# Performance work log

Measured on AMD Instinct MI355X. Metric: run time of the kernel, lower is better.

## Reference

```python
import jax, jax.numpy as jnp
import numpy as np

B, S, IN_DIM = 8, 1024, 512
EMBED_DIM, NUM_HEADS = 512, 8
HEAD_DIM = EMBED_DIM // NUM_HEADS
LN_EPS = 1e-5


def setup_inputs() -> dict:
    key = jax.random.key(0)
    k1, k2, k3 = jax.random.split(key, 3)
    x = jax.random.normal(k1, (B, S, IN_DIM), dtype=jnp.float32)
    # xavier_uniform for qkv_proj.weight [3*embed, in] and o_proj.weight [embed, embed]
    lim_qkv = float(np.sqrt(6.0 / (3 * EMBED_DIM + IN_DIM)))
    w_qkv = jax.random.uniform(k2, (3 * EMBED_DIM, IN_DIM), dtype=jnp.float32,
                               minval=-lim_qkv, maxval=lim_qkv)
    lim_o = float(np.sqrt(6.0 / (EMBED_DIM + EMBED_DIM)))
    w_o = jax.random.uniform(k3, (EMBED_DIM, EMBED_DIM), dtype=jnp.float32,
                             minval=-lim_o, maxval=lim_o)
    return {"x": x, "w_qkv": w_qkv, "w_o": w_o}


def reference(x, w_qkv, w_o):
    b, s, _ = x.shape
    # fused QKV projection: [b, s, 3*embed]
    qkv = jnp.einsum('bsi,ei->bse', x, w_qkv)
    # [b, h, s, 3*head_dim]
    qkv = qkv.reshape(b, s, NUM_HEADS, 3 * HEAD_DIM).transpose(0, 2, 1, 3)
    q, k, v = jnp.split(qkv, 3, axis=-1)
    scale = 1.0 / np.sqrt(HEAD_DIM)
    logits = jnp.einsum('bhqd,bhkd->bhqk', q, k) * scale  # [b, h, s, s]
    attn = jax.nn.softmax(logits, axis=-1)
    vals = jnp.einsum('bhqk,bhkd->bhqd', attn, v)
    vals = vals.transpose(0, 2, 1, 3).reshape(b, s, EMBED_DIM)
    o = jnp.einsum('bse,fe->bsf', vals, w_o)
    # LayerNorm over [seq, embed] jointly (fresh nn.LayerNorm([N, D]): weight=1, bias=0)
    mu = jnp.mean(o, axis=(-2, -1), keepdims=True)
    var = jnp.var(o, axis=(-2, -1), keepdims=True)
    o = (o - mu) / jnp.sqrt(var + LN_EPS)
    return o
```

## Files before the change

### kernel.cpp

```cpp
#include <hip/hip_runtime.h>
#include <hip/hip_bf16.h>
#include <math.h>

#define BB 8
#define SS 1024
#define INDIM 512
#define ED 512
#define NH 8
#define HD 64

typedef __attribute__((ext_vector_type(8))) short short8;
typedef __attribute__((ext_vector_type(4))) float f32x4;
typedef __attribute__((ext_vector_type(16))) float f32x16;
typedef unsigned short u16;

typedef __attribute__((address_space(1))) const void gv_t;
typedef __attribute__((address_space(3))) void lv_t;

static __device__ __forceinline__ u16 f2bf(float f) {
  union { float f; unsigned u; } v; v.f = f;
  unsigned r = v.u + 0x7fffu + ((v.u >> 16) & 1u);
  return (u16)(r >> 16);
}
static __device__ __forceinline__ float bf2f(u16 b) {
  union { unsigned u; float f; } v; v.u = (unsigned)b << 16; return v.f;
}

static __device__ __forceinline__ unsigned cvt_pk_bf16(float a, float b) {
  unsigned r;
  asm("v_cvt_pk_bf16_f32 %0, %1, %2" : "=v"(r) : "v"(a), "v"(b));
  return r;
}
static __device__ __forceinline__ float fast_exp2(float x) {
  float r; asm("v_exp_f32 %0, %1" : "=v"(r) : "v"(x)); return r;
}

__global__ void cvt_all(const float* __restrict__ x, const float* __restrict__ wq,
                        const float* __restrict__ wo, u16* __restrict__ xb,
                        u16* __restrict__ wqb, u16* __restrict__ wob) {
  const int n1 = 1048576;
  const int n2 = n1 + 196608;
  const int n3 = n2 + 65536;
  int i = blockIdx.x * blockDim.x + threadIdx.x;
  int stride = gridDim.x * blockDim.x;
  for (; i < n3; i += stride) {
    const float4* src; ushort4* dst; int j;
    if (i < n1)      { src = (const float4*)x;  dst = (ushort4*)xb;  j = i; }
    else if (i < n2) { src = (const float4*)wq; dst = (ushort4*)wqb; j = i - n1; }
    else             { src = (const float4*)wo; dst = (ushort4*)wob; j = i - n2; }
    float4 v = src[j];
    ushort4 o;
    o.x = f2bf(v.x); o.y = f2bf(v.y); o.z = f2bf(v.z); o.w = f2bf(v.w);
    dst[j] = o;
  }
}

template<int EPI>
__global__ __launch_bounds__(256, 2)
void gemm_nt(const u16* __restrict__ A, const u16* __restrict__ Bm, int K,
             u16* __restrict__ outB,
             u16* __restrict__ qws, u16* __restrict__ kws, u16* __restrict__ vtws,
             float2* __restrict__ partials)
{
  __shared__ u16 As[128][64];
  __shared__ u16 Bs[128][64];
  const int tid = threadIdx.x;
  const int lane = tid & 63;
  const int wv = tid >> 6;
  const int wr = wv >> 1, wc = wv & 1;
  const int bm = blockIdx.x, bn = blockIdx.y;
  const int l15 = lane & 15, lg = lane >> 4;
  const int srow8 = lane >> 3;
  const int sc8 = lane & 7;

  f32x4 acc[4][4];
  #pragma unroll
  for (int i = 0; i < 4; i++)
    #pragma unroll
    for (int j = 0; j < 4; j++) acc[i][j] = (f32x4){0.f, 0.f, 0.f, 0.f};

  for (int kk = 0; kk < K; kk += 64) {
    #pragma unroll
    for (int i = 0; i < 4; i++) {
      int r0 = (i * 4 + wv) * 8;
      int r = r0 + srow8;
      int cs = sc8 ^ (r & 7);
      const u16* ga = A + (size_t)(bm * 128 + r) * K + kk + cs * 8;
      __builtin_amdgcn_global_load_lds((gv_t*)ga, (lv_t*)&As[r0][0], 16, 0, 0);
      const u16* gb = Bm + (size_t)(bn * 128 + r) * K + kk + cs * 8;
      __builtin_amdgcn_global_load_lds((gv_t*)gb, (lv_t*)&Bs[r0][0], 16, 0, 0);
    }
    __syncthreads();
    #pragma unroll
    for (int kc = 0; kc < 2; kc++) {
      short8 af[4], bf[4];
      #pragma unroll
      for (int mi = 0; mi < 4; mi++) {
        int ra = wr * 64 + mi * 16 + l15;
        af[mi] = *(const short8*)&As[ra][((kc * 4 + lg) ^ (ra & 7)) * 8];
      }
      #pragma unroll
      for (int ni = 0; ni < 4; ni++) {
        int rb = wc * 64 + ni * 16 + l15;
        bf[ni] = *(const short8*)&Bs[rb][((kc * 4 + lg) ^ (rb & 7)) * 8];
      }
      #pragma unroll
      for (int mi = 0; mi < 4; mi++)
        #pragma unroll
        for (int ni = 0; ni < 4; ni++)
          acc[mi][ni] = __builtin_amdgcn_mfma_f32_16x16x32_bf16(af[mi], bf[ni], acc[mi][ni], 0, 0, 0);
    }
    __syncthreads();
  }

  if (EPI == 0) {
    #pragma unroll
    for (int mi = 0; mi < 4; mi++) {
      int rowg = bm * 128 + wr * 64 + mi * 16 + lg * 4;
      #pragma unroll
      for (int ni = 0; ni < 4; ni++) {
        int colg = bn * 128 + wc * 64 + ni * 16 + l15;
        #pragma unroll
        for (int r = 0; r < 4; r++) {
          int rg = rowg + r;
          float v = acc[mi][ni][r];
          int b = rg >> 10, s = rg & 1023;
          int h = colg / 192, c = colg - h * 192;
          int bh = b * 8 + h;
          if (c < 64)
            qws[((size_t)(bh * 1024 + s)) * 64 + c] = f2bf(v * 0.18033688f);
          else if (c < 128)
            kws[((size_t)(bh * 1024 + s)) * 64 + (c - 64)] = f2bf(v);
          else
            vtws[((size_t)(bh * 64 + (c - 128))) * 1024 + s] = f2bf(v);
        }
      }
    }
  } else {
    float s1 = 0.f, s2 = 0.f;
    #pragma unroll
    for (int mi = 0; mi < 4; mi++) {
      int rowg = bm * 128 + wr * 64 + mi * 16 + lg * 4;
      #pragma unroll
      for (int ni = 0; ni < 4; ni++) {
        int colg = bn * 128 + wc * 64 + ni * 16 + l15;
        #pragma unroll
        for (int r = 0; r < 4; r++) {
          float v = acc[mi][ni][r];
          s1 += v; s2 += v * v;
          outB[(size_t)(rowg + r) * 512 + colg] = f2bf(v);
        }
      }
    }
    #pragma unroll
    for (int off = 1; off < 64; off <<= 1) {
      s1 += __shfl_xor(s1, off);
      s2 += __shfl_xor(s2, off);
    }
    __shared__ float r1[4], r2[4];
    if (lane == 0) { r1[wv] = s1; r2[wv] = s2; }
    __syncthreads();
    if (tid == 0) {
      float t1 = r1[0] + r1[1] + r1[2] + r1[3];
      float t2 = r2[0] + r2[1] + r2[2] + r2[3];
      partials[bm * 4 + bn] = make_float2(t1, t2);
    }
  }
}

__global__ __launch_bounds__(512, 4)
void attn_kernel(const u16* __restrict__ qws, const u16* __restrict__ kws,
                 const u16* __restrict__ vtws, u16* __restrict__ vals)
{
  __shared__ __align__(16) u16 Ksm[2][64][72];
  __shared__ __align__(16) u16 Vsm[2][64][72];
  const int tid = threadIdx.x;
  const int lane = tid & 63;
  const int wq = tid >> 6;
  const int l31 = lane & 31;
  const int hi = lane >> 5;
  const int logical = (blockIdx.x & 7) * 32 + (blockIdx.x >> 3);
  const int bh = logical >> 2;
  const int q0 = (logical & 3) * 256;

  short8 qf[4];
  {
    const u16* qp = qws + ((size_t)bh * 1024 + q0 + wq * 32 + l31) * 64 + 8 * hi;
    #pragma unroll
    for (int j = 0; j < 4; j++) qf[j] = *(const short8*)(qp + 16 * j);
  }

  const int srow = tid >> 3;
  const int sc8 = (tid & 7) * 8;
  uint4 kreg, vreg;
  kreg = *(const uint4*)(kws + ((size_t)bh * 1024 + srow) * 64 + sc8);
  vreg = *(const uint4*)(vtws + ((size_t)(bh * 64 + srow)) * 1024 + sc8);
  *(uint4*)&Ksm[0][srow][sc8] = kreg;
  *(uint4*)&Vsm[0][srow][sc8] = vreg;
  __syncthreads();

  f32x16 o[2];
  #pragma unroll
  for (int r = 0; r < 16; r++) { o[0][r] = 0.f; o[1][r] = 0.f; }
  float m = -1e30f, l = 0.f;

  for (int t = 0; t < 16; t++) {
    const int cur = t & 1;
    if (t < 15) {
      int kv = (t + 1) * 64;
      kreg = *(const uint4*)(kws + ((size_t)bh * 1024 + kv + srow) * 64 + sc8);
      vreg = *(const uint4*)(vtws + ((size_t)(bh * 64 + srow)) * 1024 + kv + sc8);
    }

    f32x16 stv[2];
    __builtin_amdgcn_s_setprio(1);
    #pragma unroll
    for (int s2 = 0; s2 < 2; s2++) {
      f32x16 c;
      #pragma unroll
      for (int r = 0; r < 16; r++) c[r] = 0.f;
      #pragma unroll
      for (int j = 0; j < 4; j++) {
        short8 kf = *(const short8*)&Ksm[cur][s2 * 32 + l31][16 * j + 8 * hi];
        c = __builtin_amdgcn_mfma_f32_32x32x16_bf16(kf, qf[j], c, 0, 0, 0);
      }
      stv[s2] = c;
    }
    __builtin_amdgcn_s_setprio(0);

    float mx[16];
    #pragma unroll
    for (int r = 0; r < 16; r++) mx[r] = fmaxf(stv[0][r], stv[1][r]);
    #pragma unroll
    for (int w = 8; w >= 1; w >>= 1)
      #pragma unroll
      for (int r = 0; r < w; r++) mx[r] = fmaxf(mx[r], mx[r + w]);
    float pm = fmaxf(mx[0], __shfl_xor(mx[0], 32));

    if (!__all(pm - m <= 10.0f)) {
      float mn = fmaxf(m, pm);
      float al = fast_exp2(m - mn);
      m = mn; l *= al;
      #pragma unroll
      for (int reg = 0; reg < 16; reg++) {
        int qrow = (reg & 3) + 8 * (reg >> 2) + 4 * hi;
        float alo = __shfl(al, qrow);
        o[0][reg] *= alo; o[1][reg] *= alo;
      }
    }

    unsigned pk[16];
    float ps[16];
    #pragma unroll
    for (int s2 = 0; s2 < 2; s2++)
      #pragma unroll
      for (int j = 0; j < 8; j++) {
        float p0 = fast_exp2(stv[s2][2 * j] - m);
        float p1 = fast_exp2(stv[s2][2 * j + 1] - m);
        ps[s2 * 8 + j] = p0 + p1;
        pk[s2 * 8 + j] = cvt_pk_bf16(p0, p1);
      }
    #pragma unroll
    for (int w = 8; w >= 1; w >>= 1)
      #pragma unroll
      for (int r = 0; r < w; r++) ps[r] += ps[r + w];
    l += ps[0] + __shfl_xor(ps[0], 32);

    short8 pa[4];
    #pragma unroll
    for (int cc = 0; cc < 4; cc++) {
      int base = (cc >> 1) * 8 + (cc & 1) * 4;
      unsigned a0 = pk[base + 0], a2 = pk[base + 2];
      unsigned a1 = pk[base + 1], a3 = pk[base + 3];
      asm volatile("v_permlane32_swap_b32 %0, %1" : "+v"(a0), "+v"(a2));
      asm volatile("v_permlane32_swap_b32 %0, %1" : "+v"(a1), "+v"(a3));
      union { unsigned u[4]; short8 s8; } uu;
      uu.u[0] = a0; uu.u[1] = a1; uu.u[2] = a2; uu.u[3] = a3;
      pa[cc] = uu.s8;
    }

    __builtin_amdgcn_s_setprio(1);
    #pragma unroll
    for (int dh = 0; dh < 2; dh++)
      #pragma unroll
      for (int cc = 0; cc < 4; cc++) {
        short8 vf = *(const short8*)&Vsm[cur][dh * 32 + l31][16 * cc + 8 * hi];
        o[dh] = __builtin_amdgcn_mfma_f32_32x32x16_bf16(pa[cc], vf, o[dh], 0, 0, 0);
      }
    __builtin_amdgcn_s_setprio(0);

    if (t < 15) {
      *(uint4*)&Ksm[cur ^ 1][srow][sc8] = kreg;
      *(uint4*)&Vsm[cur ^ 1][srow][sc8] = vreg;
    }
    __syncthreads();
  }

  const int b = bh >> 3, h = bh & 7;
  #pragma unroll
  for (int reg = 0; reg < 16; reg++) {
    int qrow = (reg & 3) + 8 * (reg >> 2) + 4 * hi;
    float linv = 1.0f / __shfl(l, qrow);
    size_t grow = (size_t)(b * 1024 + q0 + wq * 32 + qrow) * 512 + h * 64;
    vals[grow + l31]      = f2bf(o[0][reg] * linv);
    vals[grow + 32 + l31] = f2bf(o[1][reg] * linv);
  }
}

__global__ void ln_norm3(const u16* __restrict__ ob, float* __restrict__ o,
                         const float2* __restrict__ partials) {
  const int blk = blockIdx.x;
  const int b = blk >> 8;
  const int lane = threadIdx.x & 63;
  float s1 = 0.f, s2 = 0.f;
  if (lane < 32) {
    float2 p = partials[b * 32 + lane];
    s1 = p.x; s2 = p.y;
  }
  #pragma unroll
  for (int off = 1; off < 64; off <<= 1) {
    s1 += __shfl_xor(s1, off);
    s2 += __shfl_xor(s2, off);
  }
  float mu = s1 / 524288.f;
  float rs = rsqrtf(s2 / 524288.f - mu * mu + 1e-5f);
  const size_t i = (size_t)blk * 2048 + threadIdx.x * 8;
  uint4 v = *(const uint4*)(ob + i);
  float4 o0, o1;
  o0.x = (bf2f((u16)(v.x & 0xffff)) - mu) * rs;
  o0.y = (bf2f((u16)(v.x >> 16)) - mu) * rs;
  o0.z = (bf2f((u16)(v.y & 0xffff)) - mu) * rs;
  o0.w = (bf2f((u16)(v.y >> 16)) - mu) * rs;
  o1.x = (bf2f((u16)(v.z & 0xffff)) - mu) * rs;
  o1.y = (bf2f((u16)(v.z >> 16)) - mu) * rs;
  o1.z = (bf2f((u16)(v.w & 0xffff)) - mu) * rs;
  o1.w = (bf2f((u16)(v.w >> 16)) - mu) * rs;
  *(float4*)(o + i) = o0;
  *(float4*)(o + i + 4) = o1;
}

extern "C" void kernel_launch(void* const* d_in, const int* in_sizes, int n_in,
                              void* d_out, int out_size, void* d_ws, size_t ws_size,
                              hipStream_t stream) {
  const float* x = (const float*)d_in[0];
  const float* wqkv = (const float*)d_in[1];
  const float* wo = (const float*)d_in[2];
  float* out = (float*)d_out;
  char* ws = (char*)d_ws;

  u16* xb        = (u16*)(ws + 0);
  u16* wqb       = (u16*)(ws + 8388608);
  u16* wob       = (u16*)(ws + 9961472);
  u16* qws       = (u16*)(ws + 10485760);
  u16* kws       = (u16*)(ws + 18874368);
  u16* vtws      = (u16*)(ws + 27262976);
  u16* vals      = (u16*)(ws + 35651584);
  u16* outb      = (u16*)(ws + 44040192);
  float2* parts  = (float2*)(ws + 52428800);

  cvt_all<<<1280, 256, 0, stream>>>(x, wqkv, wo, xb, wqb, wob);

  dim3 g1(64, 12);
  gemm_nt<0><<<g1, 256, 0, stream>>>(xb, wqb, 512, nullptr, qws, kws, vtws, nullptr);

  attn_kernel<<<256, 512, 0, stream>>>(qws, kws, vtws, vals);

  dim3 g2(64, 4);
  gemm_nt<1><<<g2, 256, 0, stream>>>(vals, wob, 512, outb, nullptr, nullptr, nullptr, parts);

  ln_norm3<<<2048, 256, 0, stream>>>(outb, out, parts);
}
```

Measured before the change: 81.63 us.

## Double-buffer GEMM LDS tiles with K=32 steps to overlap loads and MFMA

Restructures the projection GEMM main loop so shared-memory tiles are double-buffered. The K step drops from 64 to 32 and the swizzle changes to match. The next tile is fetched with global_load_lds while MFMAs run on the current one, which removes the serialized load-then-compute pattern and one barrier per iteration. The trade-off is smaller K chunks per iteration and a lower MFMA-to-barrier ratio, and the smaller swizzle pattern may raise LDS bank conflicts.

```diff
diff --git a/kernel.cpp b/kernel.cpp
--- a/kernel.cpp
+++ b/kernel.cpp
@@ -62,16 +62,16 @@
              u16* __restrict__ qws, u16* __restrict__ kws, u16* __restrict__ vtws,
              float2* __restrict__ partials)
 {
-  __shared__ u16 As[128][64];
-  __shared__ u16 Bs[128][64];
+  __shared__ u16 As[2][128][32];
+  __shared__ u16 Bs[2][128][32];
   const int tid = threadIdx.x;
   const int lane = tid & 63;
   const int wv = tid >> 6;
   const int wr = wv >> 1, wc = wv & 1;
   const int bm = blockIdx.x, bn = blockIdx.y;
   const int l15 = lane & 15, lg = lane >> 4;
-  const int srow8 = lane >> 3;
-  const int sc8 = lane & 7;
+  const int srow16 = lane >> 2;
+  const int sc4 = lane & 3;
 
   f32x4 acc[4][4];
   #pragma unroll
@@ -79,37 +79,50 @@
     #pragma unroll
     for (int j = 0; j < 4; j++) acc[i][j] = (f32x4){0.f, 0.f, 0.f, 0.f};
 
-  for (int kk = 0; kk < K; kk += 64) {
-    #pragma unroll
-    for (int i = 0; i < 4; i++) {
-      int r0 = (i * 4 + wv) * 8;
-      int r = r0 + srow8;
-      int cs = sc8 ^ (r & 7);
-      const u16* ga = A + (size_t)(bm * 128 + r) * K + kk + cs * 8;
-      __builtin_amdgcn_global_load_lds((gv_t*)ga, (lv_t*)&As[r0][0], 16, 0, 0);
-      const u16* gb = Bm + (size_t)(bn * 128 + r) * K + kk + cs * 8;
-      __builtin_amdgcn_global_load_lds((gv_t*)gb, (lv_t*)&Bs[r0][0], 16, 0, 0);
-    }
-    __syncthreads();
-    #pragma unroll
-    for (int kc = 0; kc < 2; kc++) {
-      short8 af[4], bf[4];
-      #pragma unroll
-      for (int mi = 0; mi < 4; mi++) {
-        int ra = wr * 64 + mi * 16 + l15;
-        af[mi] = *(const short8*)&As[ra][((kc * 4 + lg) ^ (ra & 7)) * 8];
-      }
-      #pragma unroll
-      for (int ni = 0; ni < 4; ni++) {
-        int rb = wc * 64 + ni * 16 + l15;
-        bf[ni] = *(const short8*)&Bs[rb][((kc * 4 + lg) ^ (rb & 7)) * 8];
-      }
-      #pragma unroll
-      for (int mi = 0; mi < 4; mi++)
-        #pragma unroll
-        for (int ni = 0; ni < 4; ni++)
-          acc[mi][ni] = __builtin_amdgcn_mfma_f32_16x16x32_bf16(af[mi], bf[ni], acc[mi][ni], 0, 0, 0);
-    }
+  #pragma unroll
+  for (int i = 0; i < 2; i++) {
+    int r0 = (i * 4 + wv) * 16;
+    int r = r0 + srow16;
+    int cs = sc4 ^ (r & 3);
+    const u16* ga = A + (size_t)(bm * 128 + r) * K + cs * 8;
+    __builtin_amdgcn_global_load_lds((gv_t*)ga, (lv_t*)&As[0][r0][0], 16, 0, 0);
+    const u16* gb = Bm + (size_t)(bn * 128 + r) * K + cs * 8;
+    __builtin_amdgcn_global_load_lds((gv_t*)gb, (lv_t*)&Bs[0][r0][0], 16, 0, 0);
+  }
+  __syncthreads();
+
+  const int NT = K >> 5;
+  for (int ti = 0; ti < NT; ti++) {
+    const int cur = ti & 1;
+    if (ti + 1 < NT) {
+      int kk = (ti + 1) * 32;
+      #pragma unroll
+      for (int i = 0; i < 2; i++) {
+        int r0 = (i * 4 + wv) * 16;
+        int r = r0 + srow16;
+        int cs = sc4 ^ (r & 3);
+        const u16* ga = A + (size_t)(bm * 128 + r) * K + kk + cs * 8;
+        __builtin_amdgcn_global_load_lds((gv_t*)ga, (lv_t*)&As[cur ^ 1][r0][0], 16, 0, 0);
+        const u16* gb = Bm + (size_t)(bn * 128 + r) * K + kk + cs * 8;
+        __builtin_amdgcn_global_load_lds((gv_t*)gb, (lv_t*)&Bs[cur ^ 1][r0][0], 16, 0, 0);
+      }
+    }
+    short8 af[4], bf[4];
+    #pragma unroll
+    for (int mi = 0; mi < 4; mi++) {
+      int ra = wr * 64 + mi * 16 + l15;
+      af[mi] = *(const short8*)&As[cur][ra][(lg ^ (ra & 3)) * 8];
+    }
+    #pragma unroll
+    for (int ni = 0; ni < 4; ni++) {
+      int rb = wc * 64 + ni * 16 + l15;
+      bf[ni] = *(const short8*)&Bs[cur][rb][(lg ^ (rb & 3)) * 8];
+    }
+    #pragma unroll
+    for (int mi = 0; mi < 4; mi++)
+      #pragma unroll
+      for (int ni = 0; ni < 4; ni++)
+        acc[mi][ni] = __builtin_amdgcn_mfma_f32_16x16x32_bf16(af[mi], bf[ni], acc[mi][ni], 0, 0, 0);
     __syncthreads();
   }
 
```

Measured after the change: 85.10 us. +4.3%, slower.
